# Performance work log

Measured on AMD Instinct MI355X. Metric: run time of the kernel, lower is better.

Reference implementation:

```python
import jax, jax.numpy as jnp
import numpy as np

ALPHA = 40.0
BETA = 20.0
NUM_INSTANCES = 8  # samples per class in the PK-sampled batch


def setup_inputs() -> dict:
    key = jax.random.key(0)
    n, d = 4096, 1024
    x = jax.random.normal(key, (n, d), dtype=jnp.float32)
    # L2-normalize embeddings (standard for this loss; margins 0.8/1.1 assume dist in [0,2])
    inputs = x / jnp.linalg.norm(x, axis=1, keepdims=True)
    targets = (jnp.arange(n) // NUM_INSTANCES).astype(jnp.int32)
    return {"inputs": inputs, "targets": targets}


def reference(inputs, targets):
    n = inputs.shape[0]
    # euclidean_dist: ||xi||^2 + ||xj||^2 - 2 xi.xj, clamp, sqrt
    sq = jnp.sum(inputs * inputs, axis=1)  # [n]
    dist = sq[:, None] + sq[None, :] - 2.0 * (inputs @ inputs.T)
    dist = jnp.sqrt(jnp.clip(dist, 1e-12, None))  # [n, n]

    same = targets[:, None] == targets[None, :]
    eye = jnp.eye(n, dtype=bool)
    pos_mask = same & ~eye   # positives excluding self
    neg_mask = ~same         # negatives

    exp_a = jnp.exp(ALPHA * (1.0 - dist))
    pos_logit = jnp.sum(jnp.where(pos_mask, exp_a, 0.0), axis=1)  # [n]
    neg_logit = jnp.sum(jnp.where(neg_mask, exp_a, 0.0), axis=1)  # [n]
    # a_lr is computed from .data in the original (detached)
    a_lr = jax.lax.stop_gradient(1.0 - pos_logit / (pos_logit + neg_logit))

    pos_loss = jnp.log(jnp.sum(jnp.where(pos_mask, jnp.exp(BETA * (dist - 0.8)), 0.0), axis=1))
    neg_loss = jnp.log(jnp.sum(jnp.where(neg_mask, jnp.exp(BETA * (1.1 - dist)), 0.0), axis=1))
    loss = jnp.mean(a_lr * (pos_loss + neg_loss))

    # acc_num never incremented in the original -> accuracy == 0
    accuracy = jnp.zeros((), dtype=jnp.float32)
    pos_d = jax.lax.stop_gradient(
        jnp.sum(jnp.where(pos_mask, dist, 0.0)) / jnp.sum(pos_mask))
    neg_d = jax.lax.stop_gradient(
        jnp.sum(jnp.where(neg_mask, dist, 0.0)) / jnp.sum(neg_mask))
    return jnp.stack([loss, accuracy, pos_d, neg_d])  # [4]
```

## Files before the change

kernel.cpp:

```cpp
#include <hip/hip_runtime.h>

#define N 4096
#define D 1024
#define BM 128
#define BN 128
#define BKB 128
#define NSLOT 32

typedef float floatx4 __attribute__((ext_vector_type(4)));
typedef int intx8 __attribute__((ext_vector_type(8)));
union frag8 { intx8 v; int4 q[2]; };

__global__ __launch_bounds__(256) void prep_kernel(const float* __restrict__ x,
                                                   unsigned char* __restrict__ xq,
                                                   float* __restrict__ sq,
                                                   float* __restrict__ out) {
    if (blockIdx.x == 0 && threadIdx.x == 0) {
        out[0] = 0.f; out[1] = 0.f; out[2] = 0.f; out[3] = 0.f;
    }
    int row = blockIdx.x * 4 + (threadIdx.x >> 6);
    int lane = threadIdx.x & 63;
    const float4* xr = (const float4*)(x + (size_t)row * D);
    unsigned int* qr = (unsigned int*)(xq + (size_t)row * D);
    float s = 0.f;
    #pragma unroll
    for (int j = 0; j < 4; ++j) {
        float4 v = xr[j * 64 + lane];
        s += v.x * v.x + v.y * v.y + v.z * v.z + v.w * v.w;
        unsigned int w = __builtin_amdgcn_cvt_pk_fp8_f32(v.x * 32.f, v.y * 32.f, 0, false);
        w = __builtin_amdgcn_cvt_pk_fp8_f32(v.z * 32.f, v.w * 32.f, w, true);
        qr[j * 64 + lane] = w;
    }
    #pragma unroll
    for (int sh = 1; sh < 64; sh <<= 1) s += __shfl_xor(s, sh);
    if (lane == 0) sq[row] = s;
}

__global__ __launch_bounds__(256, 2) void gemm_fused(const unsigned char* __restrict__ xq,
                                                     const float* __restrict__ sq,
                                                     float* __restrict__ colPart) {
    __shared__ __align__(16) unsigned char smem[2 * BM * BKB];

    const int bi = blockIdx.y, bj = blockIdx.x;
    const int i0 = bi * BM, j0 = bj * BN;
    const int tid = threadIdx.x;
    const int lane = tid & 63, wave = tid >> 6;
    const int wm = wave >> 1, wn = wave & 1;
    const int quad = lane >> 4, c16 = lane & 15;

    int goff[8];
    #pragma unroll
    for (int it = 0; it < 8; ++it) {
        int chunk = it * 256 + tid;
        int half = chunk >> 10;
        int c = chunk & 1023;
        int g = c >> 7, s = c & 127;
        int r = s >> 3, ch = s & 7;
        int grow = (half ? j0 : i0) + g * 16 + r;
        goff[it] = grow * D + ((ch ^ (r & 7)) << 4);
    }
    const int rowb = c16 * 128;
    const int fo0 = ((2 * quad + 0) ^ (c16 & 7)) * 16;
    const int fo1 = ((2 * quad + 1) ^ (c16 & 7)) * 16;

    floatx4 acc[4][4];
    #pragma unroll
    for (int a = 0; a < 4; ++a)
        #pragma unroll
        for (int b = 0; b < 4; ++b) acc[a][b] = (floatx4){0.f, 0.f, 0.f, 0.f};

    for (int kt = 0; kt < D; kt += BKB) {
        #pragma unroll
        for (int it = 0; it < 8; ++it) {
            const unsigned char* gp = xq + goff[it] + kt;
            unsigned char* lp = smem + (it * 256 + tid) * 16;
            __builtin_amdgcn_global_load_lds(
                (const __attribute__((address_space(1))) void*)gp,
                (__attribute__((address_space(3))) void*)lp, 16, 0, 0);
        }
        __syncthreads();

        frag8 bf[4];
        #pragma unroll
        for (int tn = 0; tn < 4; ++tn) {
            const unsigned char* bp = smem + 16384 + (wn * 4 + tn) * 2048 + rowb;
            bf[tn].q[0] = *(const int4*)(bp + fo0);
            bf[tn].q[1] = *(const int4*)(bp + fo1);
        }
        #pragma unroll
        for (int tm = 0; tm < 4; ++tm) {
            const unsigned char* ap = smem + (wm * 4 + tm) * 2048 + rowb;
            frag8 af;
            af.q[0] = *(const int4*)(ap + fo0);
            af.q[1] = *(const int4*)(ap + fo1);
            #pragma unroll
            for (int tn = 0; tn < 4; ++tn)
                acc[tm][tn] = __builtin_amdgcn_mfma_scale_f32_16x16x128_f8f6f4(
                    af.v, bf[tn].v, acc[tm][tn],
                    0, 0,
                    0, 0x7f7f7f7f,
                    0, 0x7f7f7f7f);
        }
        __syncthreads();
    }

    float sqi[4][4];
    #pragma unroll
    for (int tm = 0; tm < 4; ++tm)
        #pragma unroll
        for (int r = 0; r < 4; ++r)
            sqi[tm][r] = sq[i0 + wm * 64 + tm * 16 + quad * 4 + r];
    float sqj[4];
    #pragma unroll
    for (int tn = 0; tn < 4; ++tn)
        sqj[tn] = sq[j0 + wn * 64 + tn * 16 + c16];

    float cpa[4], cna[4], cpb[4], cnb[4], cpd[4], cnd[4];
    const bool diag = (bi == bj);
    const float DS = -0.001953125f;

    #pragma unroll
    for (int tn = 0; tn < 4; ++tn) {
        float pa = 0.f, na = 0.f, pb = 0.f, nb = 0.f, pd = 0.f, nd = 0.f;
        if (!diag) {
            #pragma unroll
            for (int tm = 0; tm < 4; ++tm)
                #pragma unroll
                for (int r = 0; r < 4; ++r) {
                    float dot = acc[tm][tn][r];
                    float dsq = fmaf(dot, DS, sqi[tm][r] + sqj[tn]);
                    float dist = sqrtf(fmaxf(dsq, 1e-12f));
                    float t = __expf(20.0f * (1.1f - dist));
                    na = fmaf(t, t, na);
                    nb += t;
                    nd += dist;
                }
        } else {
            const int gj = j0 + wn * 64 + tn * 16 + c16;
            const int gjc = gj >> 3;
            #pragma unroll
            for (int tm = 0; tm < 4; ++tm)
                #pragma unroll
                for (int r = 0; r < 4; ++r) {
                    const int gi = i0 + wm * 64 + tm * 16 + quad * 4 + r;
                    float dot = acc[tm][tn][r];
                    float dsq = fmaf(dot, DS, sqi[tm][r] + sqj[tn]);
                    float dist = sqrtf(fmaxf(dsq, 1e-12f));
                    float t = __expf(20.0f * (1.1f - dist));
                    bool same = (gi >> 3) == gjc;
                    if (same) {
                        if (gi != gj) {
                            pa = fmaf(t, t, pa);
                            pb += __expf(20.0f * (dist - 0.8f));
                            pd += dist;
                        }
                    } else {
                        na = fmaf(t, t, na);
                        nb += t;
                        nd += dist;
                    }
                }
        }
        cpa[tn] = pa; cna[tn] = na; cpb[tn] = pb;
        cnb[tn] = nb; cpd[tn] = pd; cnd[tn] = nd;
    }

    #pragma unroll
    for (int tn = 0; tn < 4; ++tn) {
        #pragma unroll
        for (int s = 16; s < 64; s <<= 1) {
            cna[tn] += __shfl_xor(cna[tn], s);
            cnb[tn] += __shfl_xor(cnb[tn], s);
            cnd[tn] += __shfl_xor(cnd[tn], s);
        }
        if (diag) {
            #pragma unroll
            for (int s = 16; s < 64; s <<= 1) {
                cpa[tn] += __shfl_xor(cpa[tn], s);
                cpb[tn] += __shfl_xor(cpb[tn], s);
                cpd[tn] += __shfl_xor(cpd[tn], s);
            }
        }
    }

    float* colBuf = (float*)smem;
    #pragma unroll
    for (int tn = 0; tn < 4; ++tn) {
        int cb = (wm * 128 + wn * 64 + tn * 16 + c16) * 6;
        colBuf[cb + 0] = cpa[tn]; colBuf[cb + 1] = cna[tn];
        colBuf[cb + 2] = cpb[tn]; colBuf[cb + 3] = cnb[tn];
        colBuf[cb + 4] = cpd[tn]; colBuf[cb + 5] = cnd[tn];
    }
    __syncthreads();

    float* dst = colPart + (size_t)bi * N * 6 + (size_t)j0 * 6;
    #pragma unroll
    for (int it = 0; it < 3; ++it) {
        int idx = it * 256 + tid;
        dst[idx] = colBuf[idx] + colBuf[768 + idx];
    }
}

__global__ __launch_bounds__(256) void reduce_finalize(const float* __restrict__ colPart,
                                                       float* __restrict__ out) {
    int j = blockIdx.x * 256 + threadIdx.x;
    float pa = 0.f, na = 0.f, pb = 0.f, nb = 0.f, pd = 0.f, nd = 0.f;
    for (int s = 0; s < NSLOT; ++s) {
        const float* p = colPart + (size_t)s * N * 6 + (size_t)j * 6;
        pa += p[0]; na += p[1]; pb += p[2];
        nb += p[3]; pd += p[4]; nd += p[5];
    }
    float a_lr = 1.0f - pa / (pa + na);
    float L = a_lr * (logf(pb) + logf(nb));

    #pragma unroll
    for (int s = 1; s < 64; s <<= 1) {
        L  += __shfl_xor(L, s);
        pd += __shfl_xor(pd, s);
        nd += __shfl_xor(nd, s);
    }
    __shared__ float r0[4], r1[4], r2[4];
    int lane = threadIdx.x & 63, w = threadIdx.x >> 6;
    if (lane == 0) { r0[w] = L; r1[w] = pd; r2[w] = nd; }
    __syncthreads();
    if (threadIdx.x == 0) {
        float Ls = r0[0] + r0[1] + r0[2] + r0[3];
        float Ps = r1[0] + r1[1] + r1[2] + r1[3];
        float Gs = r2[0] + r2[1] + r2[2] + r2[3];
        atomicAdd(out + 0, Ls / (float)N);
        atomicAdd(out + 2, Ps / ((float)N * 7.0f));
        atomicAdd(out + 3, Gs / ((float)N * (float)(N - 8)));
    }
}

extern "C" void kernel_launch(void* const* d_in, const int* in_sizes, int n_in,
                              void* d_out, int out_size, void* d_ws, size_t ws_size,
                              hipStream_t stream) {
    const float* x = (const float*)d_in[0];
    float* out = (float*)d_out;
    char* ws = (char*)d_ws;

    unsigned char* xq = (unsigned char*)ws;
    float* sq         = (float*)(ws + (size_t)N * D);
    float* colPart    = (float*)(ws + (size_t)N * D + N * 4);

    prep_kernel<<<N / 4, 256, 0, stream>>>(x, xq, sq, out);

    dim3 grid(N / BN, N / BM);
    gemm_fused<<<grid, 256, 0, stream>>>(xq, sq, colPart);

    reduce_finalize<<<N / 256, 256, 0, stream>>>(colPart, out);
}
```

Before: 101.3 us.

## Load GEMM fragments directly from global memory, dropping LDS staging

```diff
diff --git a/kernel.cpp b/kernel.cpp
--- a/kernel.cpp
+++ b/kernel.cpp
@@ -4,7 +4,6 @@
 #define D 1024
 #define BM 128
 #define BN 128
-#define BKB 128
 #define NSLOT 32
 
 typedef float floatx4 __attribute__((ext_vector_type(4)));
@@ -39,7 +38,7 @@
 __global__ __launch_bounds__(256, 2) void gemm_fused(const unsigned char* __restrict__ xq,
                                                      const float* __restrict__ sq,
                                                      float* __restrict__ colPart) {
-    __shared__ __align__(16) unsigned char smem[2 * BM * BKB];
+    __shared__ float colBuf[1536];
 
     const int bi = blockIdx.y, bj = blockIdx.x;
     const int i0 = bi * BM, j0 = bj * BN;
@@ -48,20 +47,13 @@
     const int wm = wave >> 1, wn = wave & 1;
     const int quad = lane >> 4, c16 = lane & 15;
 
-    int goff[8];
-    #pragma unroll
-    for (int it = 0; it < 8; ++it) {
-        int chunk = it * 256 + tid;
-        int half = chunk >> 10;
-        int c = chunk & 1023;
-        int g = c >> 7, s = c & 127;
-        int r = s >> 3, ch = s & 7;
-        int grow = (half ? j0 : i0) + g * 16 + r;
-        goff[it] = grow * D + ((ch ^ (r & 7)) << 4);
-    }
-    const int rowb = c16 * 128;
-    const int fo0 = ((2 * quad + 0) ^ (c16 & 7)) * 16;
-    const int fo1 = ((2 * quad + 1) ^ (c16 & 7)) * 16;
+    const unsigned char* ab[4];
+    const unsigned char* bb[4];
+    #pragma unroll
+    for (int t = 0; t < 4; ++t) {
+        ab[t] = xq + (size_t)(i0 + wm * 64 + t * 16 + c16) * D + quad * 32;
+        bb[t] = xq + (size_t)(j0 + wn * 64 + t * 16 + c16) * D + quad * 32;
+    }
 
     floatx4 acc[4][4];
     #pragma unroll
@@ -69,30 +61,19 @@
         #pragma unroll
         for (int b = 0; b < 4; ++b) acc[a][b] = (floatx4){0.f, 0.f, 0.f, 0.f};
 
-    for (int kt = 0; kt < D; kt += BKB) {
-        #pragma unroll
-        for (int it = 0; it < 8; ++it) {
-            const unsigned char* gp = xq + goff[it] + kt;
-            unsigned char* lp = smem + (it * 256 + tid) * 16;
-            __builtin_amdgcn_global_load_lds(
-                (const __attribute__((address_space(1))) void*)gp,
-                (__attribute__((address_space(3))) void*)lp, 16, 0, 0);
-        }
-        __syncthreads();
-
+    #pragma unroll
+    for (int s = 0; s < 8; ++s) {
         frag8 bf[4];
         #pragma unroll
         for (int tn = 0; tn < 4; ++tn) {
-            const unsigned char* bp = smem + 16384 + (wn * 4 + tn) * 2048 + rowb;
-            bf[tn].q[0] = *(const int4*)(bp + fo0);
-            bf[tn].q[1] = *(const int4*)(bp + fo1);
+            bf[tn].q[0] = *(const int4*)(bb[tn] + s * 128);
+            bf[tn].q[1] = *(const int4*)(bb[tn] + s * 128 + 16);
         }
         #pragma unroll
         for (int tm = 0; tm < 4; ++tm) {
-            const unsigned char* ap = smem + (wm * 4 + tm) * 2048 + rowb;
             frag8 af;
-            af.q[0] = *(const int4*)(ap + fo0);
-            af.q[1] = *(const int4*)(ap + fo1);
+            af.q[0] = *(const int4*)(ab[tm] + s * 128);
+            af.q[1] = *(const int4*)(ab[tm] + s * 128 + 16);
             #pragma unroll
             for (int tn = 0; tn < 4; ++tn)
                 acc[tm][tn] = __builtin_amdgcn_mfma_scale_f32_16x16x128_f8f6f4(
@@ -101,7 +82,6 @@
                     0, 0x7f7f7f7f,
                     0, 0x7f7f7f7f);
         }
-        __syncthreads();
     }
 
     float sqi[4][4];
@@ -183,7 +163,6 @@
         }
     }
 
-    float* colBuf = (float*)smem;
     #pragma unroll
     for (int tn = 0; tn < 4; ++tn) {
         int cb = (wm * 128 + wn * 64 + tn * 16 + c16) * 6;
```

After: 136.4 us. 34.7% more time.
